# Optimization experiments

Measured on AMD Instinct MI355X. Metric: run time of the kernel, lower is better.

## Reference

```python
import jax, jax.numpy as jnp
import numpy as np

B, S, N, F = 4, 8, 1024, 6
H, L, K, D = 64, 3, 16, 3  # hidden, layers, neighbors, num_dims
EPS = 1e-6


def setup_inputs() -> dict:
    key = jax.random.key(0)
    ks = iter(jax.random.split(key, 64))

    def w(shape, fan_in):
        return jax.random.normal(next(ks), shape, jnp.float32) / np.sqrt(fan_in)

    inp = {
        'points': jax.random.normal(next(ks), (B, S, N, F), jnp.float32),
        'w_in': w((F, H), F), 'b_in': jnp.zeros((H,), jnp.float32),
        # stacked per-layer params for the 3 PointTransformerLayers
        'Wq': w((L, H, H), H), 'bq': jnp.zeros((L, H), jnp.float32),
        'Wk': w((L, H, H), H), 'bk': jnp.zeros((L, H), jnp.float32),
        'Wv': w((L, H, H), H), 'bv': jnp.zeros((L, H), jnp.float32),
        'Wpe': w((L, D, H), D), 'bpe': jnp.zeros((L, H), jnp.float32),
        'Wpd': w((L, D, H), D), 'bpd': jnp.zeros((L, H), jnp.float32),
        'Wa': w((L, H, 1), H), 'ba': jnp.zeros((L, 1), jnp.float32),
        'Wo': w((L, H, H), H), 'bo': jnp.zeros((L, H), jnp.float32),
        'ln_s': jnp.ones((L, H), jnp.float32), 'ln_b': jnp.zeros((L, H), jnp.float32),
        # EncoderTransformerLayer params
        'Wek': w((H, H), H), 'bek': jnp.zeros((H,), jnp.float32),
        'Weq': w((H, H), H), 'beq': jnp.zeros((H,), jnp.float32),
        'Wev': w((H, H), H), 'bev': jnp.zeros((H,), jnp.float32),
        'We1': w((H, H), H), 'be1': jnp.zeros((H,), jnp.float32),
        'We2': w((H, H), H), 'be2': jnp.zeros((H,), jnp.float32),
        'ln2_s': jnp.ones((H,), jnp.float32), 'ln2_b': jnp.zeros((H,), jnp.float32),
    }
    return inp


def _layernorm(x, scale, bias):
    mu = jnp.mean(x, axis=-1, keepdims=True)
    var = jnp.var(x, axis=-1, keepdims=True)
    return (x - mu) * jax.lax.rsqrt(var + EPS) * scale + bias


def _point_layer(x, pos, Wq, bq, Wk, bk, Wv, bv, Wpe, bpe, Wpd, bpd, Wa, ba, Wo, bo):
    # x: [B,S,N,H], pos: [B,S,N,3]
    q = x @ Wq + bq
    k = x @ Wk + bk
    v = x @ Wv + bv
    pos_enc = pos @ Wpe + bpe  # [B,S,N,H]
    # pairwise squared distances: diff[i,j] = pos[i] - pos[j]
    pos_diff = pos[..., :, None, :] - pos[..., None, :, :]  # [B,S,N,N,3]
    dist = jnp.sum(pos_diff ** 2, axis=-1)                  # [B,S,N,N]
    _, nidx = jax.lax.top_k(-dist, K)                       # [B,S,N,K]

    def gather(a):  # a: [B,S,N,C] -> [B,S,N,K,C]
        return jnp.take_along_axis(a[:, :, None], nidx[..., None], axis=3)

    k_n = gather(k)
    v_n = gather(v)
    p_n = gather(pos_enc)
    qp = (q + pos_enc)[..., None, :]                        # [B,S,N,1,H]
    pd_enc = (gather(pos) - pos[..., None, :]) @ Wpd + bpd  # [B,S,N,K,H]
    scale = jnp.sqrt(jnp.float32(H))
    attn = qp * (k_n + p_n + pd_enc) / scale                # [B,S,N,K,H]
    attn = (attn @ Wa + ba).squeeze(-1)                     # [B,S,N,K]
    attn = jax.nn.softmax(attn, axis=-1)
    out = jnp.sum(attn[..., None] * v_n, axis=-2)           # [B,S,N,H]
    out = jax.nn.gelu(out @ Wo + bo)
    return x + out


def _encoder_layer(x, Wek, bek, Weq, beq, Wev, bev, We1, be1, We2, be2):
    k = x @ Wek + bek
    q = x @ Weq + beq
    v = x @ Wev + bev
    aw = jnp.einsum('bth,bsh->bts', q, k)
    aw = jax.nn.softmax(aw / jnp.sqrt(jnp.float32(H)), axis=-1)
    out = jnp.einsum('bts,bsh->bth', aw, v)
    out = jax.nn.gelu(out @ We1 + be1) @ We2 + be2
    return x + out


def reference(points, w_in, b_in, Wq, bq, Wk, bk, Wv, bv, Wpe, bpe, Wpd, bpd,
              Wa, ba, Wo, bo, ln_s, ln_b, Wek, bek, Weq, beq, Wev, bev,
              We1, be1, We2, be2, ln2_s, ln2_b):
    pos = points[..., :D]
    x = points @ w_in + b_in
    for i in range(L):
        x = _point_layer(x, pos, Wq[i], bq[i], Wk[i], bk[i], Wv[i], bv[i],
                         Wpe[i], bpe[i], Wpd[i], bpd[i], Wa[i], ba[i], Wo[i], bo[i])
        x = _layernorm(x, ln_s[i], ln_b[i])
    x = jnp.max(x, axis=-2)  # pool over points -> [B,S,H]
    x = _encoder_layer(x, Wek, bek, Weq, beq, Wev, bev, We1, be1, We2, be2)
    x = _layernorm(x, ln2_s, ln2_b)
    x = jnp.max(x, axis=-2)  # pool over seq -> [B,H]
    return x
```

## Files before the change

### kernel.cpp

```cpp
#include <hip/hip_runtime.h>
#include <cfloat>
#include <cmath>
#include <cstdint>

#define NPT   1024
#define NCL   32
#define PTOT  32768
#define HH    64
#define KNN_K 16
#define KNN_BLKS (NCL * 256)

#define RFL(x) __builtin_amdgcn_readfirstlane(x)

__device__ __forceinline__ float wave_sum64(float t) {
#pragma unroll
  for (int o = 32; o > 0; o >>= 1) t += __shfl_xor(t, o, 64);
  return t;
}

template <int NV>
__device__ __forceinline__ float mreduce(const float (&P)[NV], int lane) {
  float buf[NV];
#pragma unroll
  for (int i = 0; i < NV; ++i) buf[i] = P[i];
#pragma unroll
  for (int s = 0; (1 << s) < NV; ++s) {
    bool hi = (lane & (1 << s)) != 0;
#pragma unroll
    for (int m = 0; m < (NV >> (s + 1)); ++m) {
      float a = buf[2 * m], b = buf[2 * m + 1];
      float keep = hi ? b : a;
      float send = hi ? a : b;
      buf[m] = keep + __shfl_xor(send, 1 << s, 64);
    }
  }
  float t = buf[0];
#pragma unroll
  for (int o = NV; o < 64; o <<= 1) t += __shfl_xor(t, o, 64);
  return t;
}

__device__ __forceinline__ float gelu_f(float z) {
  float zc = 0.7978845608028654f * (z + 0.044715f * z * z * z);
  float t = __expf(2.0f * zc);
  float th = 1.0f - 2.0f / (t + 1.0f);
  return 0.5f * z * (1.0f + th);
}

__global__ __launch_bounds__(256) void k_front(
    const float* __restrict__ pts, const float* __restrict__ w_in,
    const float* __restrict__ b_in, float* __restrict__ x,
    float* __restrict__ pos4, int* __restrict__ nidx) {
  if (blockIdx.x >= KNN_BLKS) {
    int p = (blockIdx.x - KNN_BLKS) * 4 + (threadIdx.x >> 6);
    int h = threadIdx.x & 63;
    const float* pp = pts + p * 6;
    float acc = b_in[h];
#pragma unroll
    for (int f = 0; f < 6; ++f) acc += pp[f] * w_in[f * HH + h];
    x[p * HH + h] = acc;
    if (h < 4) pos4[p * 4 + h] = (h < 3) ? pp[h] : 0.0f;
    return;
  }

  __shared__ float sx[NPT], sy[NPT], sz[NPT];
  int cloud = blockIdx.x >> 8;
  int qbase = (blockIdx.x & 255) * 4;
  const float* cp = pts + (size_t)cloud * NPT * 6;
  for (int j = threadIdx.x; j < NPT; j += 256) {
    sx[j] = cp[j * 6 + 0];
    sy[j] = cp[j * 6 + 1];
    sz[j] = cp[j * 6 + 2];
  }
  __syncthreads();

  int wv = threadIdx.x >> 6;
  int lane = threadIdx.x & 63;
  int i = qbase + wv;
  float qx = sx[i], qy = sy[i], qz = sz[i];

  unsigned du[16];
#pragma unroll
  for (int c = 0; c < 16; ++c) {
    int j = c * 64 + lane;
    float dx = qx - sx[j], dy = qy - sy[j], dz = qz - sz[j];
    float d2 = __fadd_rn(__fadd_rn(__fmul_rn(dx, dx), __fmul_rn(dy, dy)),
                         __fmul_rn(dz, dz));
    du[c] = __float_as_uint(d2);
  }

  unsigned t = 0u;
  for (int bit = 30; bit >= 0; --bit) {
    unsigned tp = t | (1u << bit);
    int cnt = 0;
#pragma unroll
    for (int c = 0; c < 16; ++c)
      cnt += __popcll(__ballot(du[c] < tp));
    if (cnt <= 15) t = tp;
  }

  int obase = (cloud * NPT + i) * KNN_K;
  unsigned long long below = (1ull << lane) - 1ull;
  int slot = 0;
#pragma unroll
  for (int c = 0; c < 16; ++c) {
    bool lt = du[c] < t;
    unsigned long long m = __ballot(lt);
    if (lt) {
      int off = __popcll(m & below);
      nidx[obase + slot + off] = c * 64 + lane;
    }
    slot += __popcll(m);
  }

  int erem = KNN_K - slot;
#pragma unroll
  for (int c = 0; c < 16; ++c) {
    if (erem > 0) {
      bool eq = du[c] == t;
      unsigned long long m = __ballot(eq);
      int cnt = __popcll(m);
      int take = cnt < erem ? cnt : erem;
      if (eq) {
        int off = __popcll(m & below);
        if (off < take) nidx[obase + slot + off] = c * 64 + lane;
      }
      slot += take;
      erem -= take;
    }
  }
}

__global__ __launch_bounds__(256) void k_qkv_gemm(
    const float* __restrict__ x, const float* __restrict__ pos4,
    const float* __restrict__ Wq, const float* __restrict__ bq,
    const float* __restrict__ Wk, const float* __restrict__ bk,
    const float* __restrict__ Wv, const float* __restrict__ bv,
    const float* __restrict__ Wpe, const float* __restrict__ bpe,
    const float* __restrict__ Wpd, const float* __restrict__ bpd,
    float* __restrict__ qq, float* __restrict__ kkv) {
  int lane = threadIdx.x & 63;
  int pb = RFL(blockIdx.x * 32 + (threadIdx.x >> 6) * 8);
  const float* xw = x + (size_t)pb * HH;
  const float4* posw = reinterpret_cast<const float4*>(pos4) + pb;

  float wpe0 = Wpe[lane], wpe1 = Wpe[HH + lane], wpe2 = Wpe[2 * HH + lane];
  float wpd0 = Wpd[lane], wpd1 = Wpd[HH + lane], wpd2 = Wpd[2 * HH + lane];
  float we0 = wpe0 + wpd0, we1 = wpe1 + wpd1, we2 = wpe2 + wpd2;
  float bqq = bq[lane] + bpe[lane];
  float bkk = bk[lane] + bpe[lane] + bpd[lane];
  float bvv = bv[lane];

  float aq[8], ak[8], av[8];
#pragma unroll
  for (int p = 0; p < 8; ++p) { aq[p] = bqq; ak[p] = bkk; av[p] = bvv; }

#pragma unroll
  for (int c = 0; c < 8; ++c) {
    float wq8[8], wk8[8], wv8[8];
#pragma unroll
    for (int j = 0; j < 8; ++j) {
      int g = c * 8 + j;
      wq8[j] = Wq[g * HH + lane];
      wk8[j] = Wk[g * HH + lane];
      wv8[j] = Wv[g * HH + lane];
    }
#pragma unroll
    for (int p = 0; p < 8; ++p) {
#pragma unroll
      for (int j = 0; j < 8; ++j) {
        float xv = xw[p * HH + c * 8 + j];
        aq[p] = fmaf(xv, wq8[j], aq[p]);
        ak[p] = fmaf(xv, wk8[j], ak[p]);
        av[p] = fmaf(xv, wv8[j], av[p]);
      }
    }
  }

#pragma unroll
  for (int p = 0; p < 8; ++p) {
    float4 pp = posw[p];
    float qv = aq[p] + pp.x * wpe0 + pp.y * wpe1 + pp.z * wpe2;
    float kv = ak[p] + pp.x * we0 + pp.y * we1 + pp.z * we2;
    qq[(size_t)(pb + p) * HH + lane] = qv;
    reinterpret_cast<float2*>(kkv + ((size_t)(pb + p) << 7))[lane] =
        make_float2(kv, av[p]);
  }
}

__global__ __launch_bounds__(256) void k_attn_core(
    float* __restrict__ qq, const float* __restrict__ kkv,
    const int* __restrict__ nidx, const float* __restrict__ pos4,
    const float* __restrict__ Wpd, const float* __restrict__ Wa,
    const float* __restrict__ ba) {
  int lane = threadIdx.x & 63;
  int bid = blockIdx.x;
  int vb = (bid & 7) * (PTOT / 4 / 8) + (bid >> 3);
  int pu = RFL(vb * 4 + (threadIdx.x >> 6));
  int cbase = pu & ~(NPT - 1);

  float4 pp = reinterpret_cast<const float4*>(pos4)[pu];
  float u = qq[(size_t)pu * HH + lane] * Wa[lane] * 0.125f;
  float pdq = pp.x * Wpd[lane] + pp.y * Wpd[HH + lane] + pp.z * Wpd[2 * HH + lane];
  float C0 = wave_sum64(u * pdq) - ba[0];

  const int4* niw = reinterpret_cast<const int4*>(nidx + (size_t)pu * KNN_K);
  int nj[KNN_K];
#pragma unroll
  for (int g = 0; g < 4; ++g) {
    int4 r = niw[g];
    nj[g * 4 + 0] = r.x; nj[g * 4 + 1] = r.y;
    nj[g * 4 + 2] = r.z; nj[g * 4 + 3] = r.w;
  }

  float vj[KNN_K], P[KNN_K];
#pragma unroll
  for (int jj = 0; jj < KNN_K; ++jj) {
    float2 kv = reinterpret_cast<const float2*>(
        kkv + ((size_t)(cbase + nj[jj]) << 7))[lane];
    vj[jj] = kv.y;
    P[jj] = u * kv.x;
  }

  float T = mreduce<16>(P, lane);
  float lg = T - C0;

  float mx = lg;
#pragma unroll
  for (int o = 1; o < 16; o <<= 1) mx = fmaxf(mx, __shfl_xor(mx, o, 64));
  float e = __expf(lg - mx);
  float s = e;
#pragma unroll
  for (int o = 1; o < 16; o <<= 1) s += __shfl_xor(s, o, 64);

  float oacc = 0.f;
  int sb = lane & 48;
#pragma unroll
  for (int jj = 0; jj < KNN_K; ++jj)
    oacc = fmaf(__shfl(e, sb | jj, 64), vj[jj], oacc);

  qq[(size_t)pu * HH + lane] = oacc / s;
}

__global__ __launch_bounds__(256) void k_wo_ln(
    const float* __restrict__ outb, const float* __restrict__ Wo,
    const float* __restrict__ bo, float* __restrict__ x,
    const float* __restrict__ ln_s, const float* __restrict__ ln_b,
    float* __restrict__ partial, int do_pool) {
  __shared__ float red[4][HH];
  int lane = threadIdx.x & 63;
  int wv = threadIdx.x >> 6;
  int pb = RFL(blockIdx.x * 32 + wv * 8);
  const float* ow = outb + (size_t)pb * HH;

  float acc[8];
  float b0 = bo[lane];
#pragma unroll
  for (int p = 0; p < 8; ++p) acc[p] = b0;

#pragma unroll
  for (int c = 0; c < 8; ++c) {
    float w8[8];
#pragma unroll
    for (int j = 0; j < 8; ++j) w8[j] = Wo[(c * 8 + j) * HH + lane];
#pragma unroll
    for (int p = 0; p < 8; ++p) {
#pragma unroll
      for (int j = 0; j < 8; ++j) {
        float ov = ow[p * HH + c * 8 + j];
        acc[p] = fmaf(ov, w8[j], acc[p]);
      }
    }
  }

  float sg = ln_s[lane], bg = ln_b[lane];
  float xn[8];
#pragma unroll
  for (int p = 0; p < 8; ++p)
    xn[p] = x[(size_t)(pb + p) * HH + lane] + gelu_f(acc[p]);

  float Ts = mreduce<8>(xn, lane);
  float dd[8], sq[8];
#pragma unroll
  for (int p = 0; p < 8; ++p) {
    float mu = __shfl(Ts, p, 64) * (1.0f / HH);
    dd[p] = xn[p] - mu;
    sq[p] = dd[p] * dd[p];
  }
  float Tv = mreduce<8>(sq, lane);
  float mxp = -FLT_MAX;
#pragma unroll
  for (int p = 0; p < 8; ++p) {
    float var = __shfl(Tv, p, 64) * (1.0f / HH);
    float yv = dd[p] * rsqrtf(var + 1e-6f) * sg + bg;
    x[(size_t)(pb + p) * HH + lane] = yv;
    mxp = fmaxf(mxp, yv);
  }

  if (do_pool) {
    red[wv][lane] = mxp;
    __syncthreads();
    if (wv == 0) {
      float m = fmaxf(fmaxf(red[0][lane], red[1][lane]),
                      fmaxf(red[2][lane], red[3][lane]));
      partial[(size_t)blockIdx.x * HH + lane] = m;
    }
  }
}

__global__ __launch_bounds__(512) void k_enc(
    const float* __restrict__ partial,
    const float* __restrict__ Wek, const float* __restrict__ bek,
    const float* __restrict__ Weq, const float* __restrict__ beq,
    const float* __restrict__ Wev, const float* __restrict__ bev,
    const float* __restrict__ We1, const float* __restrict__ be1,
    const float* __restrict__ We2, const float* __restrict__ be2,
    const float* __restrict__ ln2_s, const float* __restrict__ ln2_b,
    float* __restrict__ out) {
  __shared__ float xs[8][HH], ks[8][HH], vs[8][HH], x2[8][HH];
  int b = blockIdx.x;
  int t = threadIdx.x >> 6;
  int h = threadIdx.x & 63;
  {
    int ci = b * 8 + t;
    const float* pp = partial + (size_t)ci * 32 * HH + h;
    float mx = pp[0];
#pragma unroll
    for (int c8 = 1; c8 < 32; ++c8) mx = fmaxf(mx, pp[c8 * HH]);
    xs[t][h] = mx;
  }
  __syncthreads();

  float kk = bek[h], qq = beq[h], vv = bev[h];
#pragma unroll 8
  for (int g = 0; g < HH; ++g) {
    float xv = xs[t][g];
    kk += xv * Wek[g * HH + h];
    qq += xv * Weq[g * HH + h];
    vv += xv * Wev[g * HH + h];
  }
  ks[t][h] = kk;
  vs[t][h] = vv;
  __syncthreads();

  float logit[8];
#pragma unroll
  for (int s = 0; s < 8; ++s) {
    float tt = qq * ks[s][h];
    logit[s] = wave_sum64(tt) * 0.125f;
  }
  float m = logit[0];
#pragma unroll
  for (int s = 1; s < 8; ++s) m = fmaxf(m, logit[s]);
  float ssum = 0.f;
#pragma unroll
  for (int s = 0; s < 8; ++s) { logit[s] = expf(logit[s] - m); ssum += logit[s]; }
  float o = 0.f;
#pragma unroll
  for (int s = 0; s < 8; ++s) o += (logit[s] / ssum) * vs[s][h];

  float h1 = be1[h];
#pragma unroll 8
  for (int g = 0; g < HH; ++g) h1 += __shfl(o, g, 64) * We1[g * HH + h];
  h1 = gelu_f(h1);
  float h2 = be2[h];
#pragma unroll 8
  for (int g = 0; g < HH; ++g) h2 += __shfl(h1, g, 64) * We2[g * HH + h];

  float xn = xs[t][h] + h2;
  float mu = wave_sum64(xn) * (1.0f / HH);
  float d = xn - mu;
  float var = wave_sum64(d * d) * (1.0f / HH);
  float yv = d * rsqrtf(var + 1e-6f) * ln2_s[h] + ln2_b[h];
  x2[t][h] = yv;
  __syncthreads();
  if (t == 0) {
    float mm = x2[0][h];
#pragma unroll
    for (int s = 1; s < 8; ++s) mm = fmaxf(mm, x2[s][h]);
    out[b * HH + h] = mm;
  }
}

extern "C" void kernel_launch(void* const* d_in, const int* in_sizes, int n_in,
                              void* d_out, int out_size, void* d_ws, size_t ws_size,
                              hipStream_t stream) {
  const float* points = (const float*)d_in[0];
  const float* w_in   = (const float*)d_in[1];
  const float* b_in   = (const float*)d_in[2];
  const float* Wq     = (const float*)d_in[3];
  const float* bq     = (const float*)d_in[4];
  const float* Wk     = (const float*)d_in[5];
  const float* bk     = (const float*)d_in[6];
  const float* Wv     = (const float*)d_in[7];
  const float* bv     = (const float*)d_in[8];
  const float* Wpe    = (const float*)d_in[9];
  const float* bpe    = (const float*)d_in[10];
  const float* Wpd    = (const float*)d_in[11];
  const float* bpd    = (const float*)d_in[12];
  const float* Wa     = (const float*)d_in[13];
  const float* ba     = (const float*)d_in[14];
  const float* Wo     = (const float*)d_in[15];
  const float* bo     = (const float*)d_in[16];
  const float* ln_s   = (const float*)d_in[17];
  const float* ln_b   = (const float*)d_in[18];
  const float* Wek    = (const float*)d_in[19];
  const float* bek    = (const float*)d_in[20];
  const float* Weq    = (const float*)d_in[21];
  const float* beq    = (const float*)d_in[22];
  const float* Wev    = (const float*)d_in[23];
  const float* bev    = (const float*)d_in[24];
  const float* We1    = (const float*)d_in[25];
  const float* be1    = (const float*)d_in[26];
  const float* We2    = (const float*)d_in[27];
  const float* be2    = (const float*)d_in[28];
  const float* ln2_s  = (const float*)d_in[29];
  const float* ln2_b  = (const float*)d_in[30];

  float* ws      = (float*)d_ws;
  float* pos4    = ws;
  float* xbuf    = pos4 + 4 * PTOT;
  float* qbuf    = xbuf + 64 * PTOT;
  float* kkv     = qbuf + 64 * PTOT;
  float* partial = kkv + 128 * PTOT;
  int*   nidx    = (int*)(partial + 1024 * HH);

  k_front<<<KNN_BLKS + PTOT / 4, 256, 0, stream>>>(points, w_in, b_in,
                                                   xbuf, pos4, nidx);

  for (int l = 0; l < 3; ++l) {
    k_qkv_gemm<<<PTOT / 32, 256, 0, stream>>>(xbuf, pos4,
        Wq + l * HH * HH, bq + l * HH,
        Wk + l * HH * HH, bk + l * HH,
        Wv + l * HH * HH, bv + l * HH,
        Wpe + l * 3 * HH, bpe + l * HH,
        Wpd + l * 3 * HH, bpd + l * HH,
        qbuf, kkv);
    k_attn_core<<<PTOT / 4, 256, 0, stream>>>(qbuf, kkv, nidx, pos4,
        Wpd + l * 3 * HH, Wa + l * HH, ba + l);
    k_wo_ln<<<PTOT / 32, 256, 0, stream>>>(qbuf,
        Wo + l * HH * HH, bo + l * HH, xbuf,
        ln_s + l * HH, ln_b + l * HH, partial, l == 2 ? 1 : 0);
  }

  k_enc<<<4, 512, 0, stream>>>(partial, Wek, bek, Weq, beq, Wev, bev,
                               We1, be1, We2, be2, ln2_s, ln2_b, (float*)d_out);
}
```

Baseline: 268.0 us.

## Truncate KNN radix search and resolve boundary bucket by argmin; halve GEMM points per wave

The KNN bitwise threshold search now stops after the high 16 bits. The remaining neighbors inside the boundary bucket are picked by repeated wave-wide argmin with index tie-breaking, which cuts the ballot/popcount passes. Separately, the QKV GEMM and Wo+LayerNorm kernels process 4 points per wave instead of 8, doubling grid size and the pooling partial buffer. The smaller per-wave tiles trade weight reuse for more waves and lower register pressure, while the argmin loop adds shuffle reductions per leftover neighbor.

After: 239.5 us. -10.6%, faster.

```diff
diff --git a/kernel.cpp b/kernel.cpp
--- a/kernel.cpp
+++ b/kernel.cpp
@@ -90,7 +90,8 @@
   }
 
   unsigned t = 0u;
-  for (int bit = 30; bit >= 0; --bit) {
+#pragma unroll
+  for (int bit = 30; bit >= 15; --bit) {
     unsigned tp = t | (1u << bit);
     int cnt = 0;
 #pragma unroll
@@ -114,20 +115,35 @@
   }
 
   int erem = KNN_K - slot;
-#pragma unroll
-  for (int c = 0; c < 16; ++c) {
-    if (erem > 0) {
-      bool eq = du[c] == t;
-      unsigned long long m = __ballot(eq);
-      int cnt = __popcll(m);
-      int take = cnt < erem ? cnt : erem;
-      if (eq) {
-        int off = __popcll(m & below);
-        if (off < take) nidx[obase + slot + off] = c * 64 + lane;
-      }
-      slot += take;
-      erem -= take;
-    }
+  unsigned hi_end = t + (1u << 15);
+  unsigned bu[16];
+#pragma unroll
+  for (int c = 0; c < 16; ++c)
+    bu[c] = (du[c] >= t && du[c] < hi_end) ? du[c] : 0xFFFFFFFFu;
+  for (int r2 = 0; r2 < erem; ++r2) {
+    unsigned bd = bu[0];
+    int bc = 0;
+#pragma unroll
+    for (int c = 1; c < 16; ++c) {
+      if (bu[c] < bd) { bd = bu[c]; bc = c; }
+    }
+    unsigned gd = bd;
+#pragma unroll
+    for (int o = 32; o > 0; o >>= 1) {
+      unsigned g2 = (unsigned)__shfl_xor((int)gd, o, 64);
+      gd = (g2 < gd) ? g2 : gd;
+    }
+    int myidx = bc * 64 + lane;
+    int gidx = (bd == gd) ? myidx : 0x7fffffff;
+#pragma unroll
+    for (int o = 32; o > 0; o >>= 1) {
+      int g2 = __shfl_xor(gidx, o, 64);
+      gidx = (g2 < gidx) ? g2 : gidx;
+    }
+    if (lane == 0) nidx[obase + slot + r2] = gidx;
+    int sel = (myidx == gidx) ? bc : 99;
+#pragma unroll
+    for (int c = 0; c < 16; ++c) bu[c] = (c == sel) ? 0xFFFFFFFFu : bu[c];
   }
 }
 
@@ -140,7 +156,7 @@
     const float* __restrict__ Wpd, const float* __restrict__ bpd,
     float* __restrict__ qq, float* __restrict__ kkv) {
   int lane = threadIdx.x & 63;
-  int pb = RFL(blockIdx.x * 32 + (threadIdx.x >> 6) * 8);
+  int pb = RFL(blockIdx.x * 16 + (threadIdx.x >> 6) * 4);
   const float* xw = x + (size_t)pb * HH;
   const float4* posw = reinterpret_cast<const float4*>(pos4) + pb;
 
@@ -151,9 +167,9 @@
   float bkk = bk[lane] + bpe[lane] + bpd[lane];
   float bvv = bv[lane];
 
-  float aq[8], ak[8], av[8];
-#pragma unroll
-  for (int p = 0; p < 8; ++p) { aq[p] = bqq; ak[p] = bkk; av[p] = bvv; }
+  float aq[4], ak[4], av[4];
+#pragma unroll
+  for (int p = 0; p < 4; ++p) { aq[p] = bqq; ak[p] = bkk; av[p] = bvv; }
 
 #pragma unroll
   for (int c = 0; c < 8; ++c) {
@@ -166,7 +182,7 @@
       wv8[j] = Wv[g * HH + lane];
     }
 #pragma unroll
-    for (int p = 0; p < 8; ++p) {
+    for (int p = 0; p < 4; ++p) {
 #pragma unroll
       for (int j = 0; j < 8; ++j) {
         float xv = xw[p * HH + c * 8 + j];
@@ -178,7 +194,7 @@
   }
 
 #pragma unroll
-  for (int p = 0; p < 8; ++p) {
+  for (int p = 0; p < 4; ++p) {
     float4 pp = posw[p];
     float qv = aq[p] + pp.x * wpe0 + pp.y * wpe1 + pp.z * wpe2;
     float kv = ak[p] + pp.x * we0 + pp.y * we1 + pp.z * we2;
@@ -250,13 +266,13 @@
   __shared__ float red[4][HH];
   int lane = threadIdx.x & 63;
   int wv = threadIdx.x >> 6;
-  int pb = RFL(blockIdx.x * 32 + wv * 8);
+  int pb = RFL(blockIdx.x * 16 + wv * 4);
   const float* ow = outb + (size_t)pb * HH;
 
-  float acc[8];
+  float acc[4];
   float b0 = bo[lane];
 #pragma unroll
-  for (int p = 0; p < 8; ++p) acc[p] = b0;
+  for (int p = 0; p < 4; ++p) acc[p] = b0;
 
 #pragma unroll
   for (int c = 0; c < 8; ++c) {
@@ -264,7 +280,7 @@
 #pragma unroll
     for (int j = 0; j < 8; ++j) w8[j] = Wo[(c * 8 + j) * HH + lane];
 #pragma unroll
-    for (int p = 0; p < 8; ++p) {
+    for (int p = 0; p < 4; ++p) {
 #pragma unroll
       for (int j = 0; j < 8; ++j) {
         float ov = ow[p * HH + c * 8 + j];
@@ -274,23 +290,23 @@
   }
 
   float sg = ln_s[lane], bg = ln_b[lane];
-  float xn[8];
-#pragma unroll
-  for (int p = 0; p < 8; ++p)
+  float xn[4];
+#pragma unroll
+  for (int p = 0; p < 4; ++p)
     xn[p] = x[(size_t)(pb + p) * HH + lane] + gelu_f(acc[p]);
 
-  float Ts = mreduce<8>(xn, lane);
-  float dd[8], sq[8];
-#pragma unroll
-  for (int p = 0; p < 8; ++p) {
+  float Ts = mreduce<4>(xn, lane);
+  float dd[4], sq[4];
+#pragma unroll
+  for (int p = 0; p < 4; ++p) {
     float mu = __shfl(Ts, p, 64) * (1.0f / HH);
     dd[p] = xn[p] - mu;
     sq[p] = dd[p] * dd[p];
   }
-  float Tv = mreduce<8>(sq, lane);
+  float Tv = mreduce<4>(sq, lane);
   float mxp = -FLT_MAX;
 #pragma unroll
-  for (int p = 0; p < 8; ++p) {
+  for (int p = 0; p < 4; ++p) {
     float var = __shfl(Tv, p, 64) * (1.0f / HH);
     float yv = dd[p] * rsqrtf(var + 1e-6f) * sg + bg;
     x[(size_t)(pb + p) * HH + lane] = yv;
@@ -323,10 +339,10 @@
   int h = threadIdx.x & 63;
   {
     int ci = b * 8 + t;
-    const float* pp = partial + (size_t)ci * 32 * HH + h;
+    const float* pp = partial + (size_t)ci * 64 * HH + h;
     float mx = pp[0];
 #pragma unroll
-    for (int c8 = 1; c8 < 32; ++c8) mx = fmaxf(mx, pp[c8 * HH]);
+    for (int c8 = 1; c8 < 64; ++c8) mx = fmaxf(mx, pp[c8 * HH]);
     xs[t][h] = mx;
   }
   __syncthreads();
@@ -423,13 +439,13 @@
   float* qbuf    = xbuf + 64 * PTOT;
   float* kkv     = qbuf + 64 * PTOT;
   float* partial = kkv + 128 * PTOT;
-  int*   nidx    = (int*)(partial + 1024 * HH);
+  int*   nidx    = (int*)(partial + 2048 * HH);
 
   k_front<<<KNN_BLKS + PTOT / 4, 256, 0, stream>>>(points, w_in, b_in,
                                                    xbuf, pos4, nidx);
 
   for (int l = 0; l < 3; ++l) {
-    k_qkv_gemm<<<PTOT / 32, 256, 0, stream>>>(xbuf, pos4,
+    k_qkv_gemm<<<PTOT / 16, 256, 0, stream>>>(xbuf, pos4,
         Wq + l * HH * HH, bq + l * HH,
         Wk + l * HH * HH, bk + l * HH,
         Wv + l * HH * HH, bv + l * HH,
@@ -438,7 +454,7 @@
         qbuf, kkv);
     k_attn_core<<<PTOT / 4, 256, 0, stream>>>(qbuf, kkv, nidx, pos4,
         Wpd + l * 3 * HH, Wa + l * HH, ba + l);
-    k_wo_ln<<<PTOT / 32, 256, 0, stream>>>(qbuf,
+    k_wo_ln<<<PTOT / 16, 256, 0, stream>>>(qbuf,
         Wo + l * HH * HH, bo + l * HH, xbuf,
         ln_s + l * HH, ln_b + l * HH, partial, l == 2 ? 1 : 0);
   }
```
